# Kernel tuning notes

Measured on AMD Instinct MI355X. Metric: run time of the kernel, lower is better.

Reference implementation:

```python
import jax, jax.numpy as jnp
import numpy as np

ALPHA = 20.0 / 100.0  # dt / tau
ONE_MINUS_ALPHA = 1.0 - ALPHA


def setup_inputs() -> dict:
    key = jax.random.key(0)
    k1, k2, k3 = jax.random.split(key, 3)
    T, B, I, H = 512, 128, 256, 512
    x = jax.random.normal(k1, (T, B, I), dtype=jnp.float32)
    hidden = jnp.zeros((B, H), dtype=jnp.float32)
    # torch Linear weights: [out_features, in_features], scaled like kaiming-uniform-ish
    W_in = jax.random.normal(k2, (H, I), dtype=jnp.float32) / np.sqrt(I)
    W_hh = jax.random.normal(k3, (H, H), dtype=jnp.float32) / np.sqrt(H)
    return {"x": x, "hidden": hidden, "W_in": W_in, "W_hh": W_hh}


def reference(x, hidden, W_in, W_hh):
    # Precompute input projection for all timesteps in one big matmul: [T,B,H]
    xin = jnp.einsum("tbi,hi->tbh", x, W_in)

    def step(h, xin_t):
        pre = xin_t + h @ W_hh.T  # [B,H]
        h_new = jax.nn.relu(h * ONE_MINUS_ALPHA + pre * ALPHA)
        return h_new, h_new

    h_final, output = jax.lax.scan(step, hidden, xin)
    return output, h_final
```

## Files before the change

### kernel.cpp

```cpp
#include <hip/hip_runtime.h>

typedef _Float16 half8 __attribute__((ext_vector_type(8)));
typedef float f32x4 __attribute__((ext_vector_type(4)));

#define NT 512
#define NB 128
#define NI 256
#define NH 512
#define NG 8
#define NS 8
#define FLAG_STRIDE 16

__global__ void w_transform(const float* __restrict__ Whh,
                            const float* __restrict__ Win,
                            _Float16* __restrict__ Wf_hh,
                            _Float16* __restrict__ Wf_in,
                            int* __restrict__ flags) {
  int tid = blockIdx.x * blockDim.x + threadIdx.x;
  if (tid < 32768) {
    int l = tid & 63, b = tid >> 6;
    int tk = b & 15, tn = b >> 4;
    int n = tn * 16 + (l & 15);
    int k = tk * 32 + (l >> 4) * 8;
    const float* src = Whh + (size_t)n * NH + k;
    _Float16* dst = Wf_hh + (size_t)tid * 8;
#pragma unroll
    for (int j = 0; j < 8; ++j) dst[j] = (_Float16)src[j];
  } else if (tid < 32768 + 16384) {
    int t2 = tid - 32768;
    int l = t2 & 63, b = t2 >> 6;
    int tk = b & 7, tn = b >> 3;
    int n = tn * 16 + (l & 15);
    int k = tk * 32 + (l >> 4) * 8;
    const float* src = Win + (size_t)n * NI + k;
    _Float16* dst = Wf_in + (size_t)t2 * 8;
#pragma unroll
    for (int j = 0; j < 8; ++j) dst[j] = (_Float16)src[j];
  } else if (tid < 32768 + 16384 + NG * NS * FLAG_STRIDE) {
    flags[tid - 32768 - 16384] = 0;
  }
}

__global__ __launch_bounds__(256)
void input_proj(const float* __restrict__ x,
                const _Float16* __restrict__ Wf_in,
                float* __restrict__ xin) {
  int lane = threadIdx.x & 63;
  int wv = threadIdx.x >> 6;
  int m0 = blockIdx.x * 16;
  int c = lane & 15, q = lane >> 4;
  int row = m0 + c;

  f32x4 acc[8];
#pragma unroll
  for (int i = 0; i < 8; ++i) acc[i] = (f32x4){0.f, 0.f, 0.f, 0.f};

#pragma unroll
  for (int kc = 0; kc < 8; ++kc) {
    const float4* ap = (const float4*)(x + (size_t)row * NI + kc * 32 + q * 8);
    float4 a0 = ap[0], a1 = ap[1];
    half8 a;
    a[0] = (_Float16)a0.x; a[1] = (_Float16)a0.y;
    a[2] = (_Float16)a0.z; a[3] = (_Float16)a0.w;
    a[4] = (_Float16)a1.x; a[5] = (_Float16)a1.y;
    a[6] = (_Float16)a1.z; a[7] = (_Float16)a1.w;
#pragma unroll
    for (int nt = 0; nt < 8; ++nt) {
      int tn = wv * 8 + nt;
      const half8* bp =
          (const half8*)(Wf_in + (((size_t)(tn * 8 + kc)) * 64 + lane) * 8);
      acc[nt] = __builtin_amdgcn_mfma_f32_16x16x32_f16(a, *bp, acc[nt], 0, 0, 0);
    }
  }
#pragma unroll
  for (int nt = 0; nt < 8; ++nt) {
    int n = wv * 128 + nt * 16 + c;
#pragma unroll
    for (int r = 0; r < 4; ++r) {
      int m = q * 4 + r;
      xin[(size_t)(m0 + m) * NH + n] = acc[nt][r];
    }
  }
}

__global__ __launch_bounds__(256, 1)
void recurrence(float* __restrict__ dout,
                const float* __restrict__ h0,
                const _Float16* __restrict__ Wf,
                _Float16* __restrict__ hbuf,
                int* __restrict__ flags) {
  __shared__ _Float16 h_sh[16][520];
  __shared__ _Float16 h16s[16][72];

  int g = blockIdx.x >> 3, s = blockIdx.x & 7;
  int tid = threadIdx.x, lane = tid & 63, wv = tid >> 6;
  int c = lane & 15, q = lane >> 4;
  int m0 = g * 16;
  int n0 = s * 64;
  int ncol = wv * 16 + c;

  int nt_global = s * 4 + wv;
  half8 bfrag[16];
#pragma unroll
  for (int kc = 0; kc < 16; ++kc)
    bfrag[kc] =
        *(const half8*)(Wf + (((size_t)(nt_global * 16 + kc)) * 64 + lane) * 8);

  float h32r[4];
#pragma unroll
  for (int r = 0; r < 4; ++r)
    h32r[r] = h0[(size_t)(m0 + q * 4 + r) * NH + n0 + ncol];

  for (int i = tid; i < 16 * 512; i += 256) {
    int m = i >> 9, n = i & 511;
    h_sh[m][n] = (_Float16)h0[(size_t)(m0 + m) * NH + n];
  }
  __syncthreads();

  int* fbase = flags + g * NS * FLAG_STRIDE;
  unsigned long long* hb64 = (unsigned long long*)hbuf;

  int cm = tid >> 4, cc = tid & 15;

#pragma unroll 1
  for (int t = 0; t < NT; ++t) {
    const float* xp = dout + ((size_t)t * NB + m0) * NH + n0;
    float xv[4];
#pragma unroll
    for (int r = 0; r < 4; ++r) xv[r] = xp[(size_t)(q * 4 + r) * NH + ncol];

    f32x4 acc0 = (f32x4){0.f, 0.f, 0.f, 0.f};
    f32x4 acc1 = (f32x4){0.f, 0.f, 0.f, 0.f};
#pragma unroll
    for (int kc = 0; kc < 16; kc += 2) {
      half8 a0 = *(const half8*)&h_sh[c][kc * 32 + q * 8];
      half8 a1 = *(const half8*)&h_sh[c][(kc + 1) * 32 + q * 8];
      acc0 = __builtin_amdgcn_mfma_f32_16x16x32_f16(a0, bfrag[kc], acc0, 0, 0, 0);
      acc1 = __builtin_amdgcn_mfma_f32_16x16x32_f16(a1, bfrag[kc + 1], acc1, 0, 0, 0);
    }

#pragma unroll
    for (int r = 0; r < 4; ++r) {
      int m = q * 4 + r;
      float hn = 0.8f * h32r[r] + 0.2f * (xv[r] + acc0[r] + acc1[r]);
      hn = fmaxf(hn, 0.f);
      h32r[r] = hn;
      dout[((size_t)t * NB + m0 + m) * NH + n0 + ncol] = hn;
      h16s[m][ncol] = (_Float16)hn;
      if (t == NT - 1)
        dout[(size_t)NT * NB * NH + (size_t)(m0 + m) * NH + n0 + ncol] = hn;
    }
    if (t == NT - 1) break;

    __syncthreads();

    {
      unsigned long long v = *(const unsigned long long*)&h16s[cm][cc * 4];
      __hip_atomic_store(
          hb64 + ((((size_t)(t & 1) * NB + m0 + cm) * NH + n0 + cc * 4) >> 2),
          v, __ATOMIC_RELAXED, __HIP_MEMORY_SCOPE_AGENT);
    }
    __syncthreads();

    if (tid == 0)
      __hip_atomic_store(&fbase[s * FLAG_STRIDE], t + 1, __ATOMIC_RELAXED,
                         __HIP_MEMORY_SCOPE_AGENT);
    if (wv == 0 && lane < NS) {
      while (__hip_atomic_load(&fbase[lane * FLAG_STRIDE], __ATOMIC_RELAXED,
                               __HIP_MEMORY_SCOPE_AGENT) < t + 1) {
      }
    }
    __syncthreads();

    {
      const unsigned long long* hb =
          hb64 + ((((size_t)(t & 1) * NB + m0) * NH) >> 2);
      unsigned long long v[8];
#pragma unroll
      for (int j = 0; j < 8; ++j) {
        int k = tid + j * 256;
        v[j] = __hip_atomic_load(hb + k, __ATOMIC_RELAXED,
                                 __HIP_MEMORY_SCOPE_AGENT);
      }
#pragma unroll
      for (int j = 0; j < 8; ++j) {
        int k = tid + j * 256;
        int m = k >> 7, o = k & 127;
        *(unsigned long long*)&h_sh[m][o * 4] = v[j];
      }
    }
    __syncthreads();
  }
}

extern "C" void kernel_launch(void* const* d_in, const int* in_sizes, int n_in,
                              void* d_out, int out_size, void* d_ws,
                              size_t ws_size, hipStream_t stream) {
  const float* x      = (const float*)d_in[0];
  const float* hidden = (const float*)d_in[1];
  const float* W_in   = (const float*)d_in[2];
  const float* W_hh   = (const float*)d_in[3];
  float* out = (float*)d_out;

  _Float16* Wf_hh = (_Float16*)d_ws;
  _Float16* Wf_in = Wf_hh + (size_t)NH * NH;
  _Float16* hbuf  = Wf_in;
  int* flags = (int*)((char*)d_ws + (size_t)NH * NH * 2 + (size_t)NH * NI * 2);

  w_transform<<<196, 256, 0, stream>>>(W_hh, W_in, Wf_hh, Wf_in, flags);
  input_proj<<<(NT * NB) / 16, 256, 0, stream>>>(x, Wf_in, out);

  void* args[] = {(void*)&out, (void*)&hidden, (void*)&Wf_hh, (void*)&hbuf,
                  (void*)&flags};
  hipLaunchCooperativeKernel((void*)recurrence, dim3(NG * NS), dim3(256), args,
                             0, stream);
}
```

Measured before the change: 1.322 ms.

## Replace flag barrier with sign-bit tagged data polling and double-buffered LDS

Drops the per-step flag store and spin-wait. Each step's fp16 hidden values are written to the exchange buffer with a phase pattern in their sign bits, which is possible because ReLU outputs are non-negative. Consumers poll the data words directly until the pattern matches, which removes one global round trip and two block barriers per timestep, and the LDS hidden buffer is double-buffered to allow this. It also prefetches the next step's input projection and retiles input_proj to 64 rows per block so each weight fragment is reused across four row tiles. The risks are the 0xFF memset pattern interacting with the phase bits, and relying on relaxed atomics for ordering.

```diff
diff --git a/kernel.cpp b/kernel.cpp
--- a/kernel.cpp
+++ b/kernel.cpp
@@ -9,13 +9,13 @@
 #define NH 512
 #define NG 8
 #define NS 8
-#define FLAG_STRIDE 16
+
+#define SIGN_MASK 0x8000800080008000ULL
 
 __global__ void w_transform(const float* __restrict__ Whh,
                             const float* __restrict__ Win,
                             _Float16* __restrict__ Wf_hh,
-                            _Float16* __restrict__ Wf_in,
-                            int* __restrict__ flags) {
+                            _Float16* __restrict__ Wf_in) {
   int tid = blockIdx.x * blockDim.x + threadIdx.x;
   if (tid < 32768) {
     int l = tid & 63, b = tid >> 6;
@@ -26,7 +26,7 @@
     _Float16* dst = Wf_hh + (size_t)tid * 8;
 #pragma unroll
     for (int j = 0; j < 8; ++j) dst[j] = (_Float16)src[j];
-  } else if (tid < 32768 + 16384) {
+  } else {
     int t2 = tid - 32768;
     int l = t2 & 63, b = t2 >> 6;
     int tk = b & 7, tn = b >> 3;
@@ -36,61 +36,68 @@
     _Float16* dst = Wf_in + (size_t)t2 * 8;
 #pragma unroll
     for (int j = 0; j < 8; ++j) dst[j] = (_Float16)src[j];
-  } else if (tid < 32768 + 16384 + NG * NS * FLAG_STRIDE) {
-    flags[tid - 32768 - 16384] = 0;
-  }
-}
-
-__global__ __launch_bounds__(256)
+  }
+}
+
+__global__ __launch_bounds__(256, 1)
 void input_proj(const float* __restrict__ x,
                 const _Float16* __restrict__ Wf_in,
                 float* __restrict__ xin) {
   int lane = threadIdx.x & 63;
   int wv = threadIdx.x >> 6;
-  int m0 = blockIdx.x * 16;
+  int m0 = blockIdx.x * 64;
   int c = lane & 15, q = lane >> 4;
-  int row = m0 + c;
-
-  f32x4 acc[8];
-#pragma unroll
-  for (int i = 0; i < 8; ++i) acc[i] = (f32x4){0.f, 0.f, 0.f, 0.f};
+
+  f32x4 acc[4][8];
+#pragma unroll
+  for (int mt = 0; mt < 4; ++mt)
+#pragma unroll
+    for (int nt = 0; nt < 8; ++nt) acc[mt][nt] = (f32x4){0.f, 0.f, 0.f, 0.f};
 
 #pragma unroll
   for (int kc = 0; kc < 8; ++kc) {
-    const float4* ap = (const float4*)(x + (size_t)row * NI + kc * 32 + q * 8);
-    float4 a0 = ap[0], a1 = ap[1];
-    half8 a;
-    a[0] = (_Float16)a0.x; a[1] = (_Float16)a0.y;
-    a[2] = (_Float16)a0.z; a[3] = (_Float16)a0.w;
-    a[4] = (_Float16)a1.x; a[5] = (_Float16)a1.y;
-    a[6] = (_Float16)a1.z; a[7] = (_Float16)a1.w;
+    half8 b[8];
+#pragma unroll
+    for (int nt = 0; nt < 8; ++nt)
+      b[nt] = *(const half8*)(Wf_in +
+               (((size_t)((wv * 8 + nt) * 8 + kc)) * 64 + lane) * 8);
+#pragma unroll
+    for (int mt = 0; mt < 4; ++mt) {
+      int row = m0 + mt * 16 + c;
+      const float4* ap =
+          (const float4*)(x + (size_t)row * NI + kc * 32 + q * 8);
+      float4 a0 = ap[0], a1 = ap[1];
+      half8 a;
+      a[0] = (_Float16)a0.x; a[1] = (_Float16)a0.y;
+      a[2] = (_Float16)a0.z; a[3] = (_Float16)a0.w;
+      a[4] = (_Float16)a1.x; a[5] = (_Float16)a1.y;
+      a[6] = (_Float16)a1.z; a[7] = (_Float16)a1.w;
+#pragma unroll
+      for (int nt = 0; nt < 8; ++nt)
+        acc[mt][nt] =
+            __builtin_amdgcn_mfma_f32_16x16x32_f16(a, b[nt], acc[mt][nt], 0, 0, 0);
+    }
+  }
+#pragma unroll
+  for (int mt = 0; mt < 4; ++mt)
 #pragma unroll
     for (int nt = 0; nt < 8; ++nt) {
-      int tn = wv * 8 + nt;
-      const half8* bp =
-          (const half8*)(Wf_in + (((size_t)(tn * 8 + kc)) * 64 + lane) * 8);
-      acc[nt] = __builtin_amdgcn_mfma_f32_16x16x32_f16(a, *bp, acc[nt], 0, 0, 0);
-    }
-  }
-#pragma unroll
-  for (int nt = 0; nt < 8; ++nt) {
-    int n = wv * 128 + nt * 16 + c;
-#pragma unroll
-    for (int r = 0; r < 4; ++r) {
-      int m = q * 4 + r;
-      xin[(size_t)(m0 + m) * NH + n] = acc[nt][r];
-    }
-  }
+      int n = wv * 128 + nt * 16 + c;
+#pragma unroll
+      for (int r = 0; r < 4; ++r) {
+        int m = mt * 16 + q * 4 + r;
+        xin[(size_t)(m0 + m) * NH + n] = acc[mt][nt][r];
+      }
+    }
 }
 
 __global__ __launch_bounds__(256, 1)
 void recurrence(float* __restrict__ dout,
                 const float* __restrict__ h0,
                 const _Float16* __restrict__ Wf,
-                _Float16* __restrict__ hbuf,
-                int* __restrict__ flags) {
-  __shared__ _Float16 h_sh[16][520];
-  __shared__ _Float16 h16s[16][72];
+                _Float16* __restrict__ hbuf) {
+  __shared__ _Float16 h_sh[2][16][520];
+  __shared__ unsigned short h16s[16][72];
 
   int g = blockIdx.x >> 3, s = blockIdx.x & 7;
   int tid = threadIdx.x, lane = tid & 63, wv = tid >> 6;
@@ -113,30 +120,39 @@
 
   for (int i = tid; i < 16 * 512; i += 256) {
     int m = i >> 9, n = i & 511;
-    h_sh[m][n] = (_Float16)h0[(size_t)(m0 + m) * NH + n];
+    h_sh[0][m][n] = (_Float16)h0[(size_t)(m0 + m) * NH + n];
   }
   __syncthreads();
 
-  int* fbase = flags + g * NS * FLAG_STRIDE;
   unsigned long long* hb64 = (unsigned long long*)hbuf;
-
   int cm = tid >> 4, cc = tid & 15;
+
+  float xv[4];
+  {
+    const float* xp = dout + (size_t)m0 * NH + n0;
+#pragma unroll
+    for (int r = 0; r < 4; ++r) xv[r] = xp[(size_t)(q * 4 + r) * NH + ncol];
+  }
 
 #pragma unroll 1
   for (int t = 0; t < NT; ++t) {
-    const float* xp = dout + ((size_t)t * NB + m0) * NH + n0;
-    float xv[4];
-#pragma unroll
-    for (int r = 0; r < 4; ++r) xv[r] = xp[(size_t)(q * 4 + r) * NH + ncol];
+    int p = t & 1;
 
     f32x4 acc0 = (f32x4){0.f, 0.f, 0.f, 0.f};
     f32x4 acc1 = (f32x4){0.f, 0.f, 0.f, 0.f};
 #pragma unroll
     for (int kc = 0; kc < 16; kc += 2) {
-      half8 a0 = *(const half8*)&h_sh[c][kc * 32 + q * 8];
-      half8 a1 = *(const half8*)&h_sh[c][(kc + 1) * 32 + q * 8];
+      half8 a0 = *(const half8*)&h_sh[p][c][kc * 32 + q * 8];
+      half8 a1 = *(const half8*)&h_sh[p][c][(kc + 1) * 32 + q * 8];
       acc0 = __builtin_amdgcn_mfma_f32_16x16x32_f16(a0, bfrag[kc], acc0, 0, 0, 0);
       acc1 = __builtin_amdgcn_mfma_f32_16x16x32_f16(a1, bfrag[kc + 1], acc1, 0, 0, 0);
+    }
+
+    float xvn[4];
+    {
+      const float* xp = dout + ((size_t)(t + 1) * NB + m0) * NH + n0;
+#pragma unroll
+      for (int r = 0; r < 4; ++r) xvn[r] = xp[(size_t)(q * 4 + r) * NH + ncol];
     }
 
 #pragma unroll
@@ -146,50 +162,49 @@
       hn = fmaxf(hn, 0.f);
       h32r[r] = hn;
       dout[((size_t)t * NB + m0 + m) * NH + n0 + ncol] = hn;
-      h16s[m][ncol] = (_Float16)hn;
+      h16s[m][ncol] =
+          (unsigned short)(__builtin_bit_cast(unsigned short, (_Float16)hn) &
+                           0x7FFFu);
       if (t == NT - 1)
         dout[(size_t)NT * NB * NH + (size_t)(m0 + m) * NH + n0 + ncol] = hn;
     }
     if (t == NT - 1) break;
 
     __syncthreads();
+
+    unsigned long long pat = ((t >> 1) & 1) ? SIGN_MASK : 0ULL;
 
     {
       unsigned long long v = *(const unsigned long long*)&h16s[cm][cc * 4];
       __hip_atomic_store(
-          hb64 + ((((size_t)(t & 1) * NB + m0 + cm) * NH + n0 + cc * 4) >> 2),
-          v, __ATOMIC_RELAXED, __HIP_MEMORY_SCOPE_AGENT);
-    }
-    __syncthreads();
-
-    if (tid == 0)
-      __hip_atomic_store(&fbase[s * FLAG_STRIDE], t + 1, __ATOMIC_RELAXED,
-                         __HIP_MEMORY_SCOPE_AGENT);
-    if (wv == 0 && lane < NS) {
-      while (__hip_atomic_load(&fbase[lane * FLAG_STRIDE], __ATOMIC_RELAXED,
-                               __HIP_MEMORY_SCOPE_AGENT) < t + 1) {
-      }
-    }
-    __syncthreads();
+          hb64 + ((((size_t)p * NB + m0 + cm) * NH + n0 + cc * 4) >> 2),
+          v | pat, __ATOMIC_RELAXED, __HIP_MEMORY_SCOPE_AGENT);
+    }
 
     {
-      const unsigned long long* hb =
-          hb64 + ((((size_t)(t & 1) * NB + m0) * NH) >> 2);
+      unsigned long long* hb = hb64 + ((((size_t)p * NB + m0) * NH) >> 2);
       unsigned long long v[8];
 #pragma unroll
+      for (int j = 0; j < 8; ++j)
+        v[j] = __hip_atomic_load(hb + tid + j * 256, __ATOMIC_RELAXED,
+                                 __HIP_MEMORY_SCOPE_AGENT);
+#pragma unroll
       for (int j = 0; j < 8; ++j) {
-        int k = tid + j * 256;
-        v[j] = __hip_atomic_load(hb + k, __ATOMIC_RELAXED,
-                                 __HIP_MEMORY_SCOPE_AGENT);
+        while ((v[j] & SIGN_MASK) != pat)
+          v[j] = __hip_atomic_load(hb + tid + j * 256, __ATOMIC_RELAXED,
+                                   __HIP_MEMORY_SCOPE_AGENT);
       }
 #pragma unroll
       for (int j = 0; j < 8; ++j) {
         int k = tid + j * 256;
         int m = k >> 7, o = k & 127;
-        *(unsigned long long*)&h_sh[m][o * 4] = v[j];
+        *(unsigned long long*)&h_sh[p ^ 1][m][o * 4] = v[j] & ~SIGN_MASK;
       }
     }
     __syncthreads();
+
+#pragma unroll
+    for (int r = 0; r < 4; ++r) xv[r] = xvn[r];
   }
 }
 
@@ -205,13 +220,12 @@
   _Float16* Wf_hh = (_Float16*)d_ws;
   _Float16* Wf_in = Wf_hh + (size_t)NH * NH;
   _Float16* hbuf  = Wf_in;
-  int* flags = (int*)((char*)d_ws + (size_t)NH * NH * 2 + (size_t)NH * NI * 2);
-
-  w_transform<<<196, 256, 0, stream>>>(W_hh, W_in, Wf_hh, Wf_in, flags);
-  input_proj<<<(NT * NB) / 16, 256, 0, stream>>>(x, Wf_in, out);
-
-  void* args[] = {(void*)&out, (void*)&hidden, (void*)&Wf_hh, (void*)&hbuf,
-                  (void*)&flags};
+
+  w_transform<<<192, 256, 0, stream>>>(W_hh, W_in, Wf_hh, Wf_in);
+  input_proj<<<(NT * NB) / 64, 256, 0, stream>>>(x, Wf_in, out);
+  hipMemsetAsync(hbuf, 0xFF, (size_t)2 * NB * NH * 2, stream);
+
+  void* args[] = {(void*)&out, (void*)&hidden, (void*)&Wf_hh, (void*)&hbuf};
   hipLaunchCooperativeKernel((void*)recurrence, dim3(NG * NS), dim3(256), args,
                              0, stream);
 }
```

Measured after the change: 2.026 ms. 53.2% more time.
